# Kernel optimization log

Hardware: AMD Instinct MI355X
Metric: run time of the kernel (lower is better)

## Reference

```python
import jax, jax.numpy as jnp
import numpy as np

N, D = 4096, 1024

def setup_inputs() -> dict:
    key = jax.random.key(0)
    ks = jax.random.split(key, 7)
    s = 1.0 / np.sqrt(D)
    return {
        "x": jax.random.normal(ks[0], (N, D), dtype=jnp.float32),
        "Wq": jax.random.uniform(ks[1], (D, D), jnp.float32, -s, s),
        "bq": jax.random.uniform(ks[2], (D,), jnp.float32, -s, s),
        "Wk": jax.random.uniform(ks[3], (D, D), jnp.float32, -s, s),
        "bk": jax.random.uniform(ks[4], (D,), jnp.float32, -s, s),
        "Wv": jax.random.uniform(ks[5], (D, D), jnp.float32, -s, s),
        "bv": jax.random.uniform(ks[6], (D,), jnp.float32, -s, s),
    }

def reference(x, Wq, bq, Wk, bk, Wv, bv):
    # Linear layers: y = x @ W^T + b (torch convention, W is [out, in]; here square)
    Q = x @ Wq.T + bq  # [N, D]
    K = x @ Wk.T + bk  # [N, D]
    V = x @ Wv.T + bv  # [N, D]
    scores = (Q @ K.T) / jnp.sqrt(jnp.asarray(x.shape[-1], x.dtype))  # [N, N]
    attn = jax.nn.softmax(scores, axis=-1)
    return attn @ V  # [N, D]
```

## Files before the change

### kernel.cpp

```cpp
#include <hip/hip_runtime.h>


#define N_TOK 4096
#define DDIM  1024

typedef short s16x4 __attribute__((ext_vector_type(4)));
typedef short s16x8 __attribute__((ext_vector_type(8)));
typedef float f32x4 __attribute__((ext_vector_type(4)));

#define VMCNT0() asm volatile("s_waitcnt vmcnt(0)" ::: "memory")
#define VMCNT6() asm volatile("s_waitcnt vmcnt(6)" ::: "memory")
#define VMCNT8() asm volatile("s_waitcnt vmcnt(8)" ::: "memory")
#define LGKMCNT0() asm volatile("s_waitcnt lgkmcnt(0)" ::: "memory")
#define BARRIER() do { asm volatile("" ::: "memory"); \
                       __builtin_amdgcn_s_barrier();  \
                       asm volatile("" ::: "memory"); } while (0)

__device__ inline short f2b(float f) {
  unsigned int u = __float_as_uint(f);
  unsigned int r = (u + 0x7FFFu + ((u >> 16) & 1u)) >> 16;
  return (short)(unsigned short)r;
}

__device__ __forceinline__ void gld_lds16(const short* g, short* l) {
  __builtin_amdgcn_global_load_lds(
      (const __attribute__((address_space(1))) unsigned int*)g,
      (__attribute__((address_space(3))) unsigned int*)l, 16, 0, 0);
}

__device__ __forceinline__ void xcd_remap(int gx, int& bx, int& by) {
  const int L = by * gx + bx;
  const int g = L & 7, h = L >> 3;
  by = g * 4 + (h & 3);
  bx = h >> 2;
}
__device__ __forceinline__ void xcd_remap16(int gx, int& bx, int& by) {
  const int L = by * gx + bx;
  const int g = L & 7, h = L >> 3;
  by = g * 2 + (h & 1);
  bx = h >> 1;
}

template<int BM, int BN, int BK, int MODE>
constexpr int lds_shorts() {
  return (MODE == 3 && BN * 136 > BM * BK + BN * BK) ? BN * 136
                                                     : BM * BK + BN * BK;
}

template<int BM, int BN, int BK, int MODE>
__device__ __forceinline__ void gemm_core(
    const short* __restrict__ A, const short* __restrict__ B,
    void* __restrict__ C, float* __restrict__ aux, short* smem,
    int K, int ld, int ldc, float scale, int row0, int col0)
{
  constexpr int WM = BM / 2, WN = BN / 2, AI = WM / 16, AJ = WN / 16;
  constexpr int CPR = BK / 8;
  constexpr int MASK = CPR - 1;
  constexpr int CA = BM * CPR / 256;
  constexpr int CB = BN * CPR / 256;
  constexpr int NH = BK / 32;
  short* As = smem;
  short* Bs = smem + BM * BK;

  const int tid  = threadIdx.x;
  const int wave = tid >> 6, lane = tid & 63;
  const int wm = wave >> 1, wn = wave & 1;
  const int quad = lane >> 4, lr = lane & 15;

  f32x4 acc[AI][AJ];
  #pragma unroll
  for (int i = 0; i < AI; i++)
    #pragma unroll
    for (int j = 0; j < AJ; j++) acc[i][j] = {0.f, 0.f, 0.f, 0.f};

  for (int kk = 0; kk < K; kk += BK) {
    __syncthreads();
    #pragma unroll
    for (int c = 0; c < CA; c++) {
      const int id = c * 256 + wave * 64 + lane;
      const int r = id / CPR, slot = id & MASK;
      const int q = slot ^ (r & MASK);
      gld_lds16(A + (size_t)(row0 + r) * ld + kk + q * 8,
                &As[(c * 256 + wave * 64) * 8]);
    }
    #pragma unroll
    for (int c = 0; c < CB; c++) {
      const int id = c * 256 + wave * 64 + lane;
      const int r = id / CPR, slot = id & MASK;
      const int q = slot ^ (r & MASK);
      gld_lds16(B + (size_t)(col0 + r) * ld + kk + q * 8,
                &Bs[(c * 256 + wave * 64) * 8]);
    }
    __syncthreads();

    #pragma unroll
    for (int h = 0; h < NH; h++) {
      s16x8 af[AI], bf[AJ];
      #pragma unroll
      for (int i = 0; i < AI; i++) {
        const int row = wm * WM + i * 16 + lr;
        const int ch = (h * 4 + quad) ^ (row & MASK);
        af[i] = *reinterpret_cast<const s16x8*>(&As[(row * CPR + ch) * 8]);
      }
      #pragma unroll
      for (int j = 0; j < AJ; j++) {
        const int row = wn * WN + j * 16 + lr;
        const int ch = (h * 4 + quad) ^ (row & MASK);
        bf[j] = *reinterpret_cast<const s16x8*>(&Bs[(row * CPR + ch) * 8]);
      }
      #pragma unroll
      for (int i = 0; i < AI; i++)
        #pragma unroll
        for (int j = 0; j < AJ; j++)
          acc[i][j] = __builtin_amdgcn_mfma_f32_16x16x32_bf16(af[i], bf[j], acc[i][j], 0, 0, 0);
    }
  }

  if constexpr (MODE == 0) {
    float bb[AJ];
    #pragma unroll
    for (int j = 0; j < AJ; j++) bb[j] = aux[col0 + wn * WN + j * 16 + lr];
    #pragma unroll
    for (int i = 0; i < AI; i++) {
      const int r0 = row0 + wm * WM + i * 16 + quad * 4;
      #pragma unroll
      for (int j = 0; j < AJ; j++) {
        const int c = col0 + wn * WN + j * 16 + lr;
        #pragma unroll
        for (int r = 0; r < 4; r++)
          ((short*)C)[(size_t)(r0 + r) * ldc + c] = f2b(acc[i][j][r] * scale + bb[j]);
      }
    }
  } else {
    float bb[AJ];
    #pragma unroll
    for (int j = 0; j < AJ; j++) bb[j] = aux[col0 + wn * WN + j * 16 + lr];
    __syncthreads();
    short* trans = smem;
    #pragma unroll
    for (int i = 0; i < AI; i++) {
      const int rl = wm * WM + i * 16 + quad * 4;
      #pragma unroll
      for (int j = 0; j < AJ; j++) {
        const int cl = wn * WN + j * 16 + lr;
        s16x4 v;
        #pragma unroll
        for (int r = 0; r < 4; r++) v[r] = f2b(acc[i][j][r] * scale + bb[j]);
        *reinterpret_cast<s16x4*>(&trans[cl * 136 + rl]) = v;
      }
    }
    __syncthreads();
    #pragma unroll
    for (int s = 0; s < BM * BN / 8 / 256; s++) {
      const int u = s * 256 + tid;
      const int cc = u >> (31 - __builtin_clz(BM / 8));
      const int seg = u & (BM / 8 - 1);
      s16x8 v = *reinterpret_cast<const s16x8*>(&trans[cc * 136 + seg * 8]);
      *reinterpret_cast<s16x8*>(
          &((short*)C)[(size_t)(cc + col0) * ldc + row0 + seg * 8]) = v;
    }
  }
}

#define XU  (N_TOK * DDIM / 8)
#define WU  (DDIM * DDIM / 8)
#define NCVT ((XU + 3 * WU) / 256)
__global__ __launch_bounds__(256)
void cvt_all(const float* __restrict__ x,  const float* __restrict__ wq,
             const float* __restrict__ wk, const float* __restrict__ wv,
             short* __restrict__ xb, short* __restrict__ wqb,
             short* __restrict__ wkb, short* __restrict__ wvb,
             float* __restrict__ rowsum)
{
  if (blockIdx.x >= NCVT) {
    float4 z = {0.f, 0.f, 0.f, 0.f};
    float4* p = reinterpret_cast<float4*>(rowsum) + threadIdx.x * 4;
    p[0] = z; p[1] = z; p[2] = z; p[3] = z;
    return;
  }
  int gid = blockIdx.x * 256 + threadIdx.x;
  const float* src; short* dst; int off;
  if (gid < XU)               { src = x;  dst = xb;  off = gid; }
  else if (gid < XU + WU)     { src = wq; dst = wqb; off = gid - XU; }
  else if (gid < XU + 2 * WU) { src = wk; dst = wkb; off = gid - XU - WU; }
  else                        { src = wv; dst = wvb; off = gid - XU - 2 * WU; }
  const float4* g = reinterpret_cast<const float4*>(src) + (size_t)off * 2;
  float4 a = g[0], b = g[1];
  s16x8 o;
  o[0] = f2b(a.x); o[1] = f2b(a.y); o[2] = f2b(a.z); o[3] = f2b(a.w);
  o[4] = f2b(b.x); o[5] = f2b(b.y); o[6] = f2b(b.z); o[7] = f2b(b.w);
  reinterpret_cast<s16x8*>(dst)[off] = o;
}

__global__ __launch_bounds__(256)
void k_qkv(const short* __restrict__ xb,
           const short* __restrict__ Wqb, const short* __restrict__ Wkb,
           const short* __restrict__ Wvb,
           const float* __restrict__ bq, const float* __restrict__ bk,
           const float* __restrict__ bv,
           short* __restrict__ Qb, short* __restrict__ Kb, short* __restrict__ Vt)
{
  __shared__ short smem[lds_shorts<128, 128, 64, 3>()];
  int bx = blockIdx.x, by = blockIdx.y;
  xcd_remap(DDIM / 128, bx, by);
  if (blockIdx.z == 0) {
    gemm_core<128, 128, 64, 0>(xb, Wqb, Qb, (float*)bq, smem, DDIM, DDIM, DDIM,
                               1.0f, by * 128, bx * 128);
  } else if (blockIdx.z == 1) {
    gemm_core<128, 128, 64, 0>(xb, Wkb, Kb, (float*)bk, smem, DDIM, DDIM, DDIM,
                               1.0f, by * 128, bx * 128);
  } else {
    gemm_core<128, 128, 64, 3>(xb, Wvb, Vt, (float*)bv, smem, DDIM, DDIM, N_TOK,
                               1.0f, by * 128, bx * 128);
  }
}

__global__ __launch_bounds__(256, 2)
void k_score(const short* __restrict__ Qb, const short* __restrict__ Kb,
             short* __restrict__ SP, float* __restrict__ rowsum)
{
  constexpr int BM = 128, BN = 128, BK = 64;
  constexpr int NT = DDIM / BK;
  __shared__ short smem[2][(BM + BN) * BK];

  int bx = blockIdx.x, by = blockIdx.y;
  xcd_remap(32, bx, by);
  const int row0 = by * BM, col0 = bx * BN;

  const int tid  = threadIdx.x;
  const int wave = tid >> 6, lane = tid & 63;
  const int wm = wave >> 1, wn = wave & 1;
  const int quad = lane >> 4, lr = lane & 15;

  auto stage = [&](int t, int sl) {
    #pragma unroll
    for (int c = 0; c < 8; c++) {
      const int id = c * 256 + tid;
      const int r  = id >> 3;
      const int q  = (id & 7) ^ (r & 7);
      const short* src = (r < BM)
          ? Qb + (size_t)(row0 + r) * DDIM + t * BK + q * 8
          : Kb + (size_t)(col0 + r - BM) * DDIM + t * BK + q * 8;
      gld_lds16(src, &smem[sl][(c * 256 + wave * 64) * 8]);
    }
  };

  f32x4 acc[4][4];
  #pragma unroll
  for (int i = 0; i < 4; i++)
    #pragma unroll
    for (int j = 0; j < 4; j++) acc[i][j] = {0.f, 0.f, 0.f, 0.f};

  stage(0, 0);
  stage(1, 1);
  VMCNT8();
  BARRIER();

  for (int t = 0; t < NT; t++) {
    const int sl = t & 1;
    const short* As = smem[sl];
    const short* Bs = smem[sl] + BM * BK;

    s16x8 af[2][4], bf[2][4];
    #pragma unroll
    for (int h = 0; h < 2; h++) {
      #pragma unroll
      for (int i = 0; i < 4; i++) {
        const int row = wm * 64 + i * 16 + lr;
        const int ch = (h * 4 + quad) ^ (row & 7);
        af[h][i] = *reinterpret_cast<const s16x8*>(&As[(row * 8 + ch) * 8]);
      }
      #pragma unroll
      for (int j = 0; j < 4; j++) {
        const int row = wn * 64 + j * 16 + lr;
        const int ch = (h * 4 + quad) ^ (row & 7);
        bf[h][j] = *reinterpret_cast<const s16x8*>(&Bs[(row * 8 + ch) * 8]);
      }
    }
    LGKMCNT0();
    __builtin_amdgcn_sched_barrier(0);
    BARRIER();

    const bool pf = (t + 2) < NT;
    if (pf) stage(t + 2, sl);

    __builtin_amdgcn_s_setprio(1);
    #pragma unroll
    for (int h = 0; h < 2; h++)
      #pragma unroll
      for (int i = 0; i < 4; i++)
        #pragma unroll
        for (int j = 0; j < 4; j++)
          acc[i][j] = __builtin_amdgcn_mfma_f32_16x16x32_bf16(
              af[h][i], bf[h][j], acc[i][j], 0, 0, 0);
    __builtin_amdgcn_s_setprio(0);

    if (pf) { VMCNT8(); } else { VMCNT0(); }
    BARRIER();
  }

  constexpr float scale = 0.03125f;
  #pragma unroll
  for (int i = 0; i < 4; i++) {
    const int r0 = row0 + wm * 64 + i * 16 + quad * 4;
    float ex[4][4];
    #pragma unroll
    for (int j = 0; j < 4; j++) {
      const int c = col0 + wn * 64 + j * 16 + lr;
      #pragma unroll
      for (int r = 0; r < 4; r++) {
        ex[j][r] = __expf(acc[i][j][r] * scale);
        SP[(size_t)(r0 + r) * N_TOK + c] = f2b(ex[j][r]);
      }
    }
    #pragma unroll
    for (int r = 0; r < 4; r++) {
      float s = 0.f;
      #pragma unroll
      for (int j = 0; j < 4; j++) s += ex[j][r];
      s += __shfl_xor(s, 1, 64);
      s += __shfl_xor(s, 2, 64);
      s += __shfl_xor(s, 4, 64);
      s += __shfl_xor(s, 8, 64);
      if (lr == 0) atomicAdd(&rowsum[r0 + r], s);
    }
  }
}

__global__ __launch_bounds__(256, 2)
void k_pv(const short* __restrict__ SP, const short* __restrict__ Vt,
          float* __restrict__ out, const float* __restrict__ rowsum)
{
  constexpr int BM = 128, BN = 64, BK = 64;
  constexpr int NT = N_TOK / BK;
  __shared__ short smem[2][(BM + BN) * BK];

  int bx = blockIdx.x, by = blockIdx.y;
  xcd_remap(DDIM / 64, bx, by);
  const int row0 = by * BM, col0 = bx * BN;

  const int tid  = threadIdx.x;
  const int wave = tid >> 6, lane = tid & 63;
  const int wm = wave >> 1, wn = wave & 1;
  const int quad = lane >> 4, lr = lane & 15;

  auto stage = [&](int t, int sl) {
    #pragma unroll
    for (int c = 0; c < 6; c++) {
      const int id = c * 256 + tid;
      const int r  = id >> 3;
      const int q  = (id & 7) ^ (r & 7);
      const short* src = (r < BM)
          ? SP + (size_t)(row0 + r) * N_TOK + t * BK + q * 8
          : Vt + (size_t)(col0 + r - BM) * N_TOK + t * BK + q * 8;
      gld_lds16(src, &smem[sl][(c * 256 + wave * 64) * 8]);
    }
  };

  f32x4 acc[4][2];
  #pragma unroll
  for (int i = 0; i < 4; i++)
    #pragma unroll
    for (int j = 0; j < 2; j++) acc[i][j] = {0.f, 0.f, 0.f, 0.f};

  stage(0, 0);
  stage(1, 1);
  VMCNT6();
  BARRIER();

  for (int t = 0; t < NT; t++) {
    const int sl = t & 1;
    const short* As = smem[sl];
    const short* Bs = smem[sl] + BM * BK;

    s16x8 af[2][4], bf[2][2];
    #pragma unroll
    for (int h = 0; h < 2; h++) {
      #pragma unroll
      for (int i = 0; i < 4; i++) {
        const int row = wm * 64 + i * 16 + lr;
        const int ch = (h * 4 + quad) ^ (row & 7);
        af[h][i] = *reinterpret_cast<const s16x8*>(&As[(row * 8 + ch) * 8]);
      }
      #pragma unroll
      for (int j = 0; j < 2; j++) {
        const int row = wn * 32 + j * 16 + lr;
        const int ch = (h * 4 + quad) ^ (row & 7);
        bf[h][j] = *reinterpret_cast<const s16x8*>(&Bs[(row * 8 + ch) * 8]);
      }
    }
    LGKMCNT0();
    __builtin_amdgcn_sched_barrier(0);
    BARRIER();

    const bool pf = (t + 2) < NT;
    if (pf) stage(t + 2, sl);

    __builtin_amdgcn_s_setprio(1);
    #pragma unroll
    for (int h = 0; h < 2; h++)
      #pragma unroll
      for (int i = 0; i < 4; i++)
        #pragma unroll
        for (int j = 0; j < 2; j++)
          acc[i][j] = __builtin_amdgcn_mfma_f32_16x16x32_bf16(
              af[h][i], bf[h][j], acc[i][j], 0, 0, 0);
    __builtin_amdgcn_s_setprio(0);

    if (pf) { VMCNT6(); } else { VMCNT0(); }
    BARRIER();
  }

  #pragma unroll
  for (int i = 0; i < 4; i++) {
    const int r0 = row0 + wm * 64 + i * 16 + quad * 4;
    float linv[4];
    #pragma unroll
    for (int r = 0; r < 4; r++) linv[r] = 1.0f / rowsum[r0 + r];
    #pragma unroll
    for (int j = 0; j < 2; j++) {
      const int c = col0 + wn * 32 + j * 16 + lr;
      #pragma unroll
      for (int r = 0; r < 4; r++)
        out[(size_t)(r0 + r) * DDIM + c] = acc[i][j][r] * linv[r];
    }
  }
}

extern "C" void kernel_launch(void* const* d_in, const int* in_sizes, int n_in,
                              void* d_out, int out_size, void* d_ws, size_t ws_size,
                              hipStream_t stream)
{
  const float* x  = (const float*)d_in[0];
  const float* Wq = (const float*)d_in[1];
  const float* bq = (const float*)d_in[2];
  const float* Wk = (const float*)d_in[3];
  const float* bk = (const float*)d_in[4];
  const float* Wv = (const float*)d_in[5];
  const float* bv = (const float*)d_in[6];
  float* out = (float*)d_out;

  char* ws = (char*)d_ws;
  const size_t MB = 1024 * 1024;
  short* Qb  = (short*)(ws + 0 * MB);
  short* Kb  = (short*)(ws + 8 * MB);
  short* Vt  = (short*)(ws + 24 * MB);
  short* SP  = (short*)(ws + 32 * MB);
  short* xb  = (short*)(ws + 32 * MB);
  short* Wqb = (short*)(ws + 40 * MB);
  short* Wkb = (short*)(ws + 42 * MB);
  short* Wvb = (short*)(ws + 44 * MB);
  float* rowsum = (float*)(ws + 64 * MB);

  dim3 b256(256);

  cvt_all<<<dim3(NCVT + 1), b256, 0, stream>>>(
      x, Wq, Wk, Wv, xb, Wqb, Wkb, Wvb, rowsum);

  k_qkv<<<dim3(DDIM / 128, N_TOK / 128, 3), b256, 0, stream>>>(
      xb, Wqb, Wkb, Wvb, bq, bk, bv, Qb, Kb, Vt);

  k_score<<<dim3(32, 32), b256, 0, stream>>>(Qb, Kb, SP, rowsum);

  k_pv<<<dim3(DDIM / 64, N_TOK / 128), b256, 0, stream>>>(
      SP, Vt, out, rowsum);
}
```

Before: 200.0 us.

## Double-buffer QKV projection GEMM with async global-to-LDS prefetch

```diff
diff --git a/kernel.cpp b/kernel.cpp
--- a/kernel.cpp
+++ b/kernel.cpp
@@ -34,130 +34,130 @@
   by = g * 4 + (h & 3);
   bx = h >> 2;
 }
-__device__ __forceinline__ void xcd_remap16(int gx, int& bx, int& by) {
-  const int L = by * gx + bx;
-  const int g = L & 7, h = L >> 3;
-  by = g * 2 + (h & 1);
-  bx = h >> 1;
-}
-
-template<int BM, int BN, int BK, int MODE>
-constexpr int lds_shorts() {
-  return (MODE == 3 && BN * 136 > BM * BK + BN * BK) ? BN * 136
-                                                     : BM * BK + BN * BK;
-}
-
-template<int BM, int BN, int BK, int MODE>
-__device__ __forceinline__ void gemm_core(
+
+template<int MODE>
+__device__ __forceinline__ void gemm_pipe128(
     const short* __restrict__ A, const short* __restrict__ B,
-    void* __restrict__ C, float* __restrict__ aux, short* smem,
+    void* __restrict__ C, const float* __restrict__ aux,
+    short (*smem)[(128 + 128) * 64],
     int K, int ld, int ldc, float scale, int row0, int col0)
 {
-  constexpr int WM = BM / 2, WN = BN / 2, AI = WM / 16, AJ = WN / 16;
-  constexpr int CPR = BK / 8;
-  constexpr int MASK = CPR - 1;
-  constexpr int CA = BM * CPR / 256;
-  constexpr int CB = BN * CPR / 256;
-  constexpr int NH = BK / 32;
-  short* As = smem;
-  short* Bs = smem + BM * BK;
+  constexpr int BM = 128, BN = 128, BK = 64;
+  const int NT = K / BK;
 
   const int tid  = threadIdx.x;
   const int wave = tid >> 6, lane = tid & 63;
   const int wm = wave >> 1, wn = wave & 1;
   const int quad = lane >> 4, lr = lane & 15;
 
-  f32x4 acc[AI][AJ];
+  auto stage = [&](int t, int sl) {
+    #pragma unroll
+    for (int c = 0; c < 8; c++) {
+      const int id = c * 256 + tid;
+      const int r  = id >> 3;
+      const int q  = (id & 7) ^ (r & 7);
+      const short* src = (r < BM)
+          ? A + (size_t)(row0 + r) * ld + t * BK + q * 8
+          : B + (size_t)(col0 + r - BM) * ld + t * BK + q * 8;
+      gld_lds16(src, &smem[sl][(c * 256 + wave * 64) * 8]);
+    }
+  };
+
+  f32x4 acc[4][4];
   #pragma unroll
-  for (int i = 0; i < AI; i++)
-    #pragma unroll
-    for (int j = 0; j < AJ; j++) acc[i][j] = {0.f, 0.f, 0.f, 0.f};
-
-  for (int kk = 0; kk < K; kk += BK) {
-    __syncthreads();
-    #pragma unroll
-    for (int c = 0; c < CA; c++) {
-      const int id = c * 256 + wave * 64 + lane;
-      const int r = id / CPR, slot = id & MASK;
-      const int q = slot ^ (r & MASK);
-      gld_lds16(A + (size_t)(row0 + r) * ld + kk + q * 8,
-                &As[(c * 256 + wave * 64) * 8]);
-    }
-    #pragma unroll
-    for (int c = 0; c < CB; c++) {
-      const int id = c * 256 + wave * 64 + lane;
-      const int r = id / CPR, slot = id & MASK;
-      const int q = slot ^ (r & MASK);
-      gld_lds16(B + (size_t)(col0 + r) * ld + kk + q * 8,
-                &Bs[(c * 256 + wave * 64) * 8]);
-    }
-    __syncthreads();
-
-    #pragma unroll
-    for (int h = 0; h < NH; h++) {
-      s16x8 af[AI], bf[AJ];
-      #pragma unroll
-      for (int i = 0; i < AI; i++) {
-        const int row = wm * WM + i * 16 + lr;
-        const int ch = (h * 4 + quad) ^ (row & MASK);
-        af[i] = *reinterpret_cast<const s16x8*>(&As[(row * CPR + ch) * 8]);
-      }
-      #pragma unroll
-      for (int j = 0; j < AJ; j++) {
-        const int row = wn * WN + j * 16 + lr;
-        const int ch = (h * 4 + quad) ^ (row & MASK);
-        bf[j] = *reinterpret_cast<const s16x8*>(&Bs[(row * CPR + ch) * 8]);
-      }
-      #pragma unroll
-      for (int i = 0; i < AI; i++)
+  for (int i = 0; i < 4; i++)
+    #pragma unroll
+    for (int j = 0; j < 4; j++) acc[i][j] = {0.f, 0.f, 0.f, 0.f};
+
+  stage(0, 0);
+  stage(1, 1);
+  VMCNT8();
+  BARRIER();
+
+  for (int t = 0; t < NT; t++) {
+    const int sl = t & 1;
+    const short* As = smem[sl];
+    const short* Bs = smem[sl] + BM * BK;
+
+    s16x8 af[2][4], bf[2][4];
+    #pragma unroll
+    for (int h = 0; h < 2; h++) {
+      #pragma unroll
+      for (int i = 0; i < 4; i++) {
+        const int row = wm * 64 + i * 16 + lr;
+        const int ch = (h * 4 + quad) ^ (row & 7);
+        af[h][i] = *reinterpret_cast<const s16x8*>(&As[(row * 8 + ch) * 8]);
+      }
+      #pragma unroll
+      for (int j = 0; j < 4; j++) {
+        const int row = wn * 64 + j * 16 + lr;
+        const int ch = (h * 4 + quad) ^ (row & 7);
+        bf[h][j] = *reinterpret_cast<const s16x8*>(&Bs[(row * 8 + ch) * 8]);
+      }
+    }
+    LGKMCNT0();
+    __builtin_amdgcn_sched_barrier(0);
+    BARRIER();
+
+    const bool pf = (t + 2) < NT;
+    if (pf) stage(t + 2, sl);
+
+    __builtin_amdgcn_s_setprio(1);
+    #pragma unroll
+    for (int h = 0; h < 2; h++)
+      #pragma unroll
+      for (int i = 0; i < 4; i++)
         #pragma unroll
-        for (int j = 0; j < AJ; j++)
-          acc[i][j] = __builtin_amdgcn_mfma_f32_16x16x32_bf16(af[i], bf[j], acc[i][j], 0, 0, 0);
-    }
+        for (int j = 0; j < 4; j++)
+          acc[i][j] = __builtin_amdgcn_mfma_f32_16x16x32_bf16(
+              af[h][i], bf[h][j], acc[i][j], 0, 0, 0);
+    __builtin_amdgcn_s_setprio(0);
+
+    if (pf) { VMCNT8(); } else { VMCNT0(); }
+    BARRIER();
   }
 
   if constexpr (MODE == 0) {
-    float bb[AJ];
-    #pragma unroll
-    for (int j = 0; j < AJ; j++) bb[j] = aux[col0 + wn * WN + j * 16 + lr];
-    #pragma unroll
-    for (int i = 0; i < AI; i++) {
-      const int r0 = row0 + wm * WM + i * 16 + quad * 4;
-      #pragma unroll
-      for (int j = 0; j < AJ; j++) {
-        const int c = col0 + wn * WN + j * 16 + lr;
+    float bb[4];
+    #pragma unroll
+    for (int j = 0; j < 4; j++) bb[j] = aux[col0 + wn * 64 + j * 16 + lr];
+    #pragma unroll
+    for (int i = 0; i < 4; i++) {
+      const int r0 = row0 + wm * 64 + i * 16 + quad * 4;
+      #pragma unroll
+      for (int j = 0; j < 4; j++) {
+        const int c = col0 + wn * 64 + j * 16 + lr;
         #pragma unroll
         for (int r = 0; r < 4; r++)
           ((short*)C)[(size_t)(r0 + r) * ldc + c] = f2b(acc[i][j][r] * scale + bb[j]);
       }
     }
   } else {
-    float bb[AJ];
-    #pragma unroll
-    for (int j = 0; j < AJ; j++) bb[j] = aux[col0 + wn * WN + j * 16 + lr];
-    __syncthreads();
-    short* trans = smem;
-    #pragma unroll
-    for (int i = 0; i < AI; i++) {
-      const int rl = wm * WM + i * 16 + quad * 4;
-      #pragma unroll
-      for (int j = 0; j < AJ; j++) {
-        const int cl = wn * WN + j * 16 + lr;
+    float bb[4];
+    #pragma unroll
+    for (int j = 0; j < 4; j++) bb[j] = aux[col0 + wn * 64 + j * 16 + lr];
+    short* trans = &smem[0][0];
+    #pragma unroll
+    for (int i = 0; i < 4; i++) {
+      const int rl = wm * 64 + i * 16 + quad * 4;
+      #pragma unroll
+      for (int j = 0; j < 4; j++) {
+        const int cl = wn * 64 + j * 16 + lr;
         s16x4 v;
         #pragma unroll
         for (int r = 0; r < 4; r++) v[r] = f2b(acc[i][j][r] * scale + bb[j]);
         *reinterpret_cast<s16x4*>(&trans[cl * 136 + rl]) = v;
       }
     }
-    __syncthreads();
-    #pragma unroll
-    for (int s = 0; s < BM * BN / 8 / 256; s++) {
+    BARRIER();
+    #pragma unroll
+    for (int s = 0; s < 8; s++) {
       const int u = s * 256 + tid;
-      const int cc = u >> (31 - __builtin_clz(BM / 8));
-      const int seg = u & (BM / 8 - 1);
+      const int cc = u >> 4;
+      const int seg = u & 15;
       s16x8 v = *reinterpret_cast<const s16x8*>(&trans[cc * 136 + seg * 8]);
       *reinterpret_cast<s16x8*>(
-          &((short*)C)[(size_t)(cc + col0) * ldc + row0 + seg * 8]) = v;
+          &((short*)C)[(size_t)(col0 + cc) * ldc + row0 + seg * 8]) = v;
     }
   }
 }
@@ -192,7 +192,7 @@
   reinterpret_cast<s16x8*>(dst)[off] = o;
 }
 
-__global__ __launch_bounds__(256)
+__global__ __launch_bounds__(256, 2)
 void k_qkv(const short* __restrict__ xb,
            const short* __restrict__ Wqb, const short* __restrict__ Wkb,
            const short* __restrict__ Wvb,
@@ -200,18 +200,18 @@
            const float* __restrict__ bv,
            short* __restrict__ Qb, short* __restrict__ Kb, short* __restrict__ Vt)
 {
-  __shared__ short smem[lds_shorts<128, 128, 64, 3>()];
+  __shared__ short smem[2][(128 + 128) * 64];
   int bx = blockIdx.x, by = blockIdx.y;
   xcd_remap(DDIM / 128, bx, by);
   if (blockIdx.z == 0) {
-    gemm_core<128, 128, 64, 0>(xb, Wqb, Qb, (float*)bq, smem, DDIM, DDIM, DDIM,
-                               1.0f, by * 128, bx * 128);
+    gemm_pipe128<0>(xb, Wqb, Qb, bq, smem, DDIM, DDIM, DDIM,
+                    1.0f, by * 128, bx * 128);
   } else if (blockIdx.z == 1) {
-    gemm_core<128, 128, 64, 0>(xb, Wkb, Kb, (float*)bk, smem, DDIM, DDIM, DDIM,
-                               1.0f, by * 128, bx * 128);
+    gemm_pipe128<0>(xb, Wkb, Kb, bk, smem, DDIM, DDIM, DDIM,
+                    1.0f, by * 128, bx * 128);
   } else {
-    gemm_core<128, 128, 64, 3>(xb, Wvb, Vt, (float*)bv, smem, DDIM, DDIM, N_TOK,
-                               1.0f, by * 128, bx * 128);
+    gemm_pipe128<3>(xb, Wvb, Vt, bv, smem, DDIM, DDIM, N_TOK,
+                    1.0f, by * 128, bx * 128);
   }
 }
 
```

Result: no change. 197.7 us (-1.1%).
